# Optimization experiments

Hardware: AMD Instinct MI355X
Metric: run time of the kernel (lower is better)

## Reference

```python
import jax, jax.numpy as jnp
import numpy as np

SEQ = 4096
VOCAB = 50257
IN = 1024
HID = 1024


def setup_inputs() -> dict:
    key = jax.random.key(0)
    ks = jax.random.split(key, 8)
    s = 1.0 / np.sqrt(HID).astype(np.float32)
    inputs = jax.random.randint(ks[0], (SEQ,), 0, VOCAB)
    emb = jax.random.normal(ks[1], (VOCAB, IN), jnp.float32) * 0.02
    W_ih = jax.random.uniform(ks[2], (4 * HID, IN), jnp.float32, -s, s)
    W_hh = jax.random.uniform(ks[3], (4 * HID, HID), jnp.float32, -s, s)
    b_ih = jax.random.uniform(ks[4], (4 * HID,), jnp.float32, -s, s)
    b_hh = jax.random.uniform(ks[5], (4 * HID,), jnp.float32, -s, s)
    h0 = jax.random.normal(ks[6], (HID,), jnp.float32)
    c0 = jax.random.normal(ks[7], (HID,), jnp.float32)
    return {"inputs": inputs, "emb": emb, "W_ih": W_ih, "W_hh": W_hh,
            "b_ih": b_ih, "b_hh": b_hh, "h0": h0, "c0": c0}


def _lstm_last_hidden(inputs, emb, W_ih, W_hh, b_ih, b_hh, h0, c0):
    # Embed all tokens, then precompute the input-side gate projections in
    # one big GEMM: [S, 4H]. (Fuses the per-timestep x @ W_ih.T of torch.)
    x = emb[inputs]                      # [S, IN]
    xg = x @ W_ih.T + (b_ih + b_hh)      # [S, 4H]

    def step(carry, xg_t):
        h, c = carry
        g = xg_t + W_hh @ h              # [4H], PyTorch gate order i,f,g,o
        i, f, gg, o = jnp.split(g, 4)
        i = jax.nn.sigmoid(i)
        f = jax.nn.sigmoid(f)
        gg = jnp.tanh(gg)
        o = jax.nn.sigmoid(o)
        c = f * c + i * gg
        h = o * jnp.tanh(c)
        return (h, c), None

    (h, _), _ = jax.lax.scan(step, (h0, c0), xg)
    return h                              # [HID] = out of last timestep


def reference(inputs, emb, W_ih, W_hh, b_ih, b_hh, h0, c0):
    h = _lstm_last_hidden(inputs, emb, W_ih, W_hh, b_ih, b_hh, h0, c0)
    # scores = F.log_softmax(out.view(1, -1), dim=1) -> [1, HID]
    return jax.nn.log_softmax(h[None, :], axis=1)
```

## Files before the change

kernel.cpp:

```cpp
#include <hip/hip_runtime.h>
#include <cmath>

#define SEQ   4096
#define INP   1024
#define HID   1024
#define G4    4096

__global__ __launch_bounds__(256) void xg_gemm_kernel(
    const int* __restrict__ inputs,
    const float* __restrict__ emb,
    const float* __restrict__ W_ih,
    const float* __restrict__ b_ih,
    const float* __restrict__ b_hh,
    float* __restrict__ xg)
{
    __shared__ __align__(16) float As[16][68];
    __shared__ __align__(16) float Bs[16][68];
    __shared__ int toks[64];

    const int tid = threadIdx.x;
    const int bt = blockIdx.y * 64;
    const int br = blockIdx.x * 64;

    if (tid < 64) toks[tid] = inputs[bt + tid];
    __syncthreads();

    const int tx = tid & 15;
    const int ty = tid >> 4;
    const int si = tid >> 2;
    const int sk = (tid & 3) * 4;

    float acc[4][4] = {};

    for (int kk = 0; kk < INP; kk += 16) {
        float4 av = *(const float4*)(emb  + (size_t)toks[si] * INP + kk + sk);
        float4 bv = *(const float4*)(W_ih + (size_t)(br + si) * INP + kk + sk);
        As[sk+0][si] = av.x; As[sk+1][si] = av.y; As[sk+2][si] = av.z; As[sk+3][si] = av.w;
        Bs[sk+0][si] = bv.x; Bs[sk+1][si] = bv.y; Bs[sk+2][si] = bv.z; Bs[sk+3][si] = bv.w;
        __syncthreads();
        #pragma unroll
        for (int k = 0; k < 16; ++k) {
            float4 a = *(const float4*)&As[k][ty * 4];
            float4 b = *(const float4*)&Bs[k][tx * 4];
            float ar[4] = {a.x, a.y, a.z, a.w};
            float brr[4] = {b.x, b.y, b.z, b.w};
            #pragma unroll
            for (int iy = 0; iy < 4; ++iy)
                #pragma unroll
                for (int ix = 0; ix < 4; ++ix)
                    acc[iy][ix] += ar[iy] * brr[ix];
        }
        __syncthreads();
    }

    const int r0 = br + tx * 4;
    float4 bias;
    bias.x = b_ih[r0+0] + b_hh[r0+0];
    bias.y = b_ih[r0+1] + b_hh[r0+1];
    bias.z = b_ih[r0+2] + b_hh[r0+2];
    bias.w = b_ih[r0+3] + b_hh[r0+3];
    #pragma unroll
    for (int iy = 0; iy < 4; ++iy) {
        float4 o;
        o.x = acc[iy][0] + bias.x;
        o.y = acc[iy][1] + bias.y;
        o.z = acc[iy][2] + bias.z;
        o.w = acc[iy][3] + bias.w;
        *(float4*)(xg + (size_t)(bt + ty * 4 + iy) * G4 + r0) = o;
    }
}

__device__ __forceinline__ float fast_sigmoid(float x) {
    x = fminf(fmaxf(x, -30.f), 30.f);
    return __builtin_amdgcn_rcpf(1.0f + __expf(-x));
}
__device__ __forceinline__ float fast_tanh(float x) {
    x = fminf(fmaxf(x, -15.f), 15.f);
    float e = __expf(2.0f * x);
    return (e - 1.0f) * __builtin_amdgcn_rcpf(e + 1.0f);
}

__device__ __forceinline__ unsigned long long mb_load(const unsigned long long* p) {
    return __hip_atomic_load(p, __ATOMIC_RELAXED, __HIP_MEMORY_SCOPE_AGENT);
}

template <int CTRL>
__device__ __forceinline__ float dpp_mov(float x) {
    return __int_as_float(__builtin_amdgcn_update_dpp(
        0, __float_as_int(x), CTRL, 0xF, 0xF, true));
}

__global__ __launch_bounds__(1024, 4) void lstm_kernel(
    const float* __restrict__ xg,
    const float* __restrict__ W_hh,
    const float* __restrict__ h0,
    const float* __restrict__ c0,
    unsigned long long* __restrict__ hbuf,
    float* __restrict__ out)
{
    const int w    = blockIdx.x;
    const int tid  = threadIdx.x;
    const int lane = tid & 63;
    const int wv   = tid >> 6;
    const int qq   = lane >> 4;
    const int kc   = lane & 15;
    const int j    = w * 16 + wv;

    float wreg[4][16];
    {
        #pragma unroll
        for (int q = 0; q < 4; ++q) {
            const float* wp = W_hh + (size_t)(q * HID + j) * HID + kc * 64 + qq * 16;
            #pragma unroll
            for (int m = 0; m < 4; ++m) {
                float4 v = *(const float4*)(wp + 4 * m);
                wreg[q][4*m+0] = v.x; wreg[q][4*m+1] = v.y;
                wreg[q][4*m+2] = v.z; wreg[q][4*m+3] = v.w;
            }
        }
    }

    float c = c0[j];

    if (wv == 0 && lane < 16) {
        unsigned long long pk =
            (unsigned long long)__float_as_uint(h0[w * 16 + lane]);
        __hip_atomic_store(hbuf + w * 16 + lane, pk,
                           __ATOMIC_RELAXED, __HIP_MEMORY_SCOPE_AGENT);
    }

    __shared__ __align__(16) float hs[16 * 68];
    __shared__ float xgs[64];
    __shared__ float hout[16];

    const int lofs = (tid >> 6) * 68 + (tid & 63);
    const bool hasx = (tid < 64);
    const size_t xgofs = (size_t)(tid >> 4) * HID + w * 16 + (tid & 15);
    const float* hp = hs + kc * 68 + qq * 16;

    for (int t = 0; t < SEQ; ++t) {
        const int par = t & 1;
        const unsigned long long* slot = hbuf + (size_t)par * 1024 + tid;

        float xv = 0.f;
        if (hasx) xv = xg[(size_t)t * G4 + xgofs];

        const unsigned int tg = (unsigned int)t;
        unsigned long long v;
        {
            unsigned long long p0 = mb_load(slot);
            unsigned long long p1 = mb_load(slot);
            unsigned long long p2 = mb_load(slot);
            unsigned long long p3 = mb_load(slot);
            for (;;) {
                if ((unsigned int)(p0 >> 32) == tg) { v = p0; break; }
                p0 = mb_load(slot);
                if ((unsigned int)(p1 >> 32) == tg) { v = p1; break; }
                p1 = mb_load(slot);
                if ((unsigned int)(p2 >> 32) == tg) { v = p2; break; }
                p2 = mb_load(slot);
                if ((unsigned int)(p3 >> 32) == tg) { v = p3; break; }
                p3 = mb_load(slot);
            }
        }

        hs[lofs] = __uint_as_float((unsigned int)v);
        if (hasx) xgs[tid] = xv;
        __syncthreads();

        float p[4] = {0.f, 0.f, 0.f, 0.f};
        #pragma unroll
        for (int m = 0; m < 4; ++m) {
            float4 hv = *(const float4*)(hp + 4 * m);
            #pragma unroll
            for (int q = 0; q < 4; ++q) {
                p[q] += wreg[q][4*m+0] * hv.x;
                p[q] += wreg[q][4*m+1] * hv.y;
                p[q] += wreg[q][4*m+2] * hv.z;
                p[q] += wreg[q][4*m+3] * hv.w;
            }
        }

        #pragma unroll
        for (int q = 0; q < 4; ++q) {
            p[q] += dpp_mov<0xB1>(p[q]);
            p[q] += dpp_mov<0x4E>(p[q]);
            p[q] += dpp_mov<0x124>(p[q]);
            p[q] += dpp_mov<0x128>(p[q]);
            p[q] += __shfl_xor(p[q], 16);
            p[q] += __shfl_xor(p[q], 32);
        }

        float gi = p[0] + xgs[ 0 + wv];
        float gf = p[1] + xgs[16 + wv];
        float gg = p[2] + xgs[32 + wv];
        float go = p[3] + xgs[48 + wv];

        float ig = fast_sigmoid(gi);
        float fg = fast_sigmoid(gf);
        float gc = fast_tanh(gg);
        float og = fast_sigmoid(go);
        c = fg * c + ig * gc;
        float h = og * fast_tanh(c);

        if (lane == 0) hout[wv] = h;
        __syncthreads();

        if (wv == 0 && lane < 16) {
            unsigned long long pk =
                ((unsigned long long)(unsigned int)(t + 1) << 32) |
                (unsigned long long)__float_as_uint(hout[lane]);
            __hip_atomic_store(
                hbuf + (size_t)((t + 1) & 1) * 1024 + w * 16 + lane, pk,
                __ATOMIC_RELAXED, __HIP_MEMORY_SCOPE_AGENT);
        }
    }

    if (w != 0) return;

    float a;
    {
        const unsigned int tg = (unsigned int)SEQ;
        const unsigned long long* slot = hbuf + tid;
        unsigned long long v;
        do {
            v = mb_load(slot);
        } while ((unsigned int)(v >> 32) != tg);
        a = __uint_as_float((unsigned int)v);
    }

    __shared__ float rmax[16];
    __shared__ float rsum[16];

    float lm = a;
    #pragma unroll
    for (int d = 1; d < 64; d <<= 1) lm = fmaxf(lm, __shfl_xor(lm, d));
    if (lane == 0) rmax[wv] = lm;
    __syncthreads();
    float gm = rmax[0];
    #pragma unroll
    for (int i = 1; i < 16; ++i) gm = fmaxf(gm, rmax[i]);

    float ls = expf(a - gm);
    #pragma unroll
    for (int d = 1; d < 64; d <<= 1) ls += __shfl_xor(ls, d);
    if (lane == 0) rsum[wv] = ls;
    __syncthreads();
    float tot = rsum[0];
    #pragma unroll
    for (int i = 1; i < 16; ++i) tot += rsum[i];
    const float lse = gm + logf(tot);

    out[tid] = a - lse;
}

extern "C" void kernel_launch(void* const* d_in, const int* in_sizes, int n_in,
                              void* d_out, int out_size, void* d_ws, size_t ws_size,
                              hipStream_t stream)
{
    const int*   inputs = (const int*)d_in[0];
    const float* emb    = (const float*)d_in[1];
    const float* W_ih   = (const float*)d_in[2];
    const float* W_hh   = (const float*)d_in[3];
    const float* b_ih   = (const float*)d_in[4];
    const float* b_hh   = (const float*)d_in[5];
    const float* h0     = (const float*)d_in[6];
    const float* c0     = (const float*)d_in[7];
    float* out = (float*)d_out;

    float* xg = (float*)d_ws;
    unsigned long long* hbuf =
        (unsigned long long*)((char*)d_ws + (size_t)SEQ * G4 * sizeof(float));

    dim3 g1(G4 / 64, SEQ / 64), b1(256);
    hipLaunchKernelGGL(xg_gemm_kernel, g1, b1, 0, stream,
                       inputs, emb, W_ih, b_ih, b_hh, xg);

    void* args[] = { (void*)&xg, (void*)&W_hh, (void*)&h0, (void*)&c0,
                     (void*)&hbuf, (void*)&out };
    hipLaunchCooperativeKernel((void*)lstm_kernel, dim3(64), dim3(1024),
                               args, 0u, stream);
}
```

Before: 9.456 ms.

## Spread LSTM recurrence over 256 small blocks with double-buffered smem and one barrier

The persistent recurrent kernel moves from 64 blocks of 1024 threads (16 hidden units each) to 256 blocks of 256 threads (4 hidden units each). Each thread now polls four hbuf slots and stages h into shared memory. The shared h and xg buffers are double-buffered by step parity, so the second __syncthreads per step is dropped and each wave publishes its own h. The aim is shorter block-wide barriers and more CUs working on the matvec, at the cost of more blocks polling global memory and more polling per thread.

```diff
diff --git a/kernel.cpp b/kernel.cpp
--- a/kernel.cpp
+++ b/kernel.cpp
@@ -90,7 +90,7 @@
         0, __float_as_int(x), CTRL, 0xF, 0xF, true));
 }
 
-__global__ __launch_bounds__(1024, 4) void lstm_kernel(
+__global__ __launch_bounds__(256, 1) void lstm_kernel(
     const float* __restrict__ xg,
     const float* __restrict__ W_hh,
     const float* __restrict__ h0,
@@ -104,7 +104,14 @@
     const int wv   = tid >> 6;
     const int qq   = lane >> 4;
     const int kc   = lane & 15;
-    const int j    = w * 16 + wv;
+    const int j    = w * 4 + wv;
+
+    if (lane == 0) {
+        unsigned long long pk =
+            (unsigned long long)__float_as_uint(h0[j]);
+        __hip_atomic_store(hbuf + j, pk,
+                           __ATOMIC_RELAXED, __HIP_MEMORY_SCOPE_AGENT);
+    }
 
     float wreg[4][16];
     {
@@ -122,21 +129,12 @@
 
     float c = c0[j];
 
-    if (wv == 0 && lane < 16) {
-        unsigned long long pk =
-            (unsigned long long)__float_as_uint(h0[w * 16 + lane]);
-        __hip_atomic_store(hbuf + w * 16 + lane, pk,
-                           __ATOMIC_RELAXED, __HIP_MEMORY_SCOPE_AGENT);
-    }
-
-    __shared__ __align__(16) float hs[16 * 68];
-    __shared__ float xgs[64];
-    __shared__ float hout[16];
-
-    const int lofs = (tid >> 6) * 68 + (tid & 63);
-    const bool hasx = (tid < 64);
-    const size_t xgofs = (size_t)(tid >> 4) * HID + w * 16 + (tid & 15);
-    const float* hp = hs + kc * 68 + qq * 16;
+    __shared__ __align__(16) float hs[2][16 * 68];
+    __shared__ float xgs[2][16];
+
+    const int wofs = (tid >> 6) * 68 + (tid & 63);
+    const bool hasx = (tid < 16);
+    const size_t xgofs = (size_t)(tid >> 2) * HID + w * 4 + (tid & 3);
 
     for (int t = 0; t < SEQ; ++t) {
         const int par = t & 1;
@@ -146,28 +144,27 @@
         if (hasx) xv = xg[(size_t)t * G4 + xgofs];
 
         const unsigned int tg = (unsigned int)t;
-        unsigned long long v;
-        {
-            unsigned long long p0 = mb_load(slot);
-            unsigned long long p1 = mb_load(slot);
-            unsigned long long p2 = mb_load(slot);
-            unsigned long long p3 = mb_load(slot);
-            for (;;) {
-                if ((unsigned int)(p0 >> 32) == tg) { v = p0; break; }
-                p0 = mb_load(slot);
-                if ((unsigned int)(p1 >> 32) == tg) { v = p1; break; }
-                p1 = mb_load(slot);
-                if ((unsigned int)(p2 >> 32) == tg) { v = p2; break; }
-                p2 = mb_load(slot);
-                if ((unsigned int)(p3 >> 32) == tg) { v = p3; break; }
-                p3 = mb_load(slot);
-            }
-        }
-
-        hs[lofs] = __uint_as_float((unsigned int)v);
-        if (hasx) xgs[tid] = xv;
+        unsigned long long a0 = mb_load(slot);
+        unsigned long long a1 = mb_load(slot + 256);
+        unsigned long long a2 = mb_load(slot + 512);
+        unsigned long long a3 = mb_load(slot + 768);
+        unsigned mOK = 0u;
+        while (mOK != 15u) {
+            if (!(mOK & 1u)) { if ((unsigned)(a0 >> 32) == tg) mOK |= 1u; else a0 = mb_load(slot);       }
+            if (!(mOK & 2u)) { if ((unsigned)(a1 >> 32) == tg) mOK |= 2u; else a1 = mb_load(slot + 256); }
+            if (!(mOK & 4u)) { if ((unsigned)(a2 >> 32) == tg) mOK |= 4u; else a2 = mb_load(slot + 512); }
+            if (!(mOK & 8u)) { if ((unsigned)(a3 >> 32) == tg) mOK |= 8u; else a3 = mb_load(slot + 768); }
+        }
+
+        float* hb = hs[par];
+        hb[wofs           ] = __uint_as_float((unsigned)a0);
+        hb[wofs +  4 * 68 ] = __uint_as_float((unsigned)a1);
+        hb[wofs +  8 * 68 ] = __uint_as_float((unsigned)a2);
+        hb[wofs + 12 * 68 ] = __uint_as_float((unsigned)a3);
+        if (hasx) xgs[par][tid] = xv;
         __syncthreads();
 
+        const float* hp = hb + kc * 68 + qq * 16;
         float p[4] = {0.f, 0.f, 0.f, 0.f};
         #pragma unroll
         for (int m = 0; m < 4; ++m) {
@@ -191,10 +188,10 @@
             p[q] += __shfl_xor(p[q], 32);
         }
 
-        float gi = p[0] + xgs[ 0 + wv];
-        float gf = p[1] + xgs[16 + wv];
-        float gg = p[2] + xgs[32 + wv];
-        float go = p[3] + xgs[48 + wv];
+        float gi = p[0] + xgs[par][ 0 + wv];
+        float gf = p[1] + xgs[par][ 4 + wv];
+        float gg = p[2] + xgs[par][ 8 + wv];
+        float go = p[3] + xgs[par][12 + wv];
 
         float ig = fast_sigmoid(gi);
         float fg = fast_sigmoid(gf);
@@ -203,55 +200,79 @@
         c = fg * c + ig * gc;
         float h = og * fast_tanh(c);
 
-        if (lane == 0) hout[wv] = h;
-        __syncthreads();
-
-        if (wv == 0 && lane < 16) {
+        if (lane == 0) {
             unsigned long long pk =
                 ((unsigned long long)(unsigned int)(t + 1) << 32) |
-                (unsigned long long)__float_as_uint(hout[lane]);
+                (unsigned long long)__float_as_uint(h);
             __hip_atomic_store(
-                hbuf + (size_t)((t + 1) & 1) * 1024 + w * 16 + lane, pk,
+                hbuf + (size_t)((t + 1) & 1) * 1024 + j, pk,
                 __ATOMIC_RELAXED, __HIP_MEMORY_SCOPE_AGENT);
         }
     }
 
     if (w != 0) return;
 
-    float a;
+    const unsigned int tgf = (unsigned int)SEQ;
+    float a0, a1, a2, a3;
     {
-        const unsigned int tg = (unsigned int)SEQ;
-        const unsigned long long* slot = hbuf + tid;
         unsigned long long v;
-        do {
-            v = mb_load(slot);
-        } while ((unsigned int)(v >> 32) != tg);
-        a = __uint_as_float((unsigned int)v);
+        do { v = mb_load(hbuf + tid);       } while ((unsigned)(v >> 32) != tgf);
+        a0 = __uint_as_float((unsigned)v);
+        do { v = mb_load(hbuf + tid + 256); } while ((unsigned)(v >> 32) != tgf);
+        a1 = __uint_as_float((unsigned)v);
+        do { v = mb_load(hbuf + tid + 512); } while ((unsigned)(v >> 32) != tgf);
+        a2 = __uint_as_float((unsigned)v);
+        do { v = mb_load(hbuf + tid + 768); } while ((unsigned)(v >> 32) != tgf);
+        a3 = __uint_as_float((unsigned)v);
     }
 
     __shared__ float rmax[16];
     __shared__ float rsum[16];
 
-    float lm = a;
-    #pragma unroll
-    for (int d = 1; d < 64; d <<= 1) lm = fmaxf(lm, __shfl_xor(lm, d));
-    if (lane == 0) rmax[wv] = lm;
+    float m0 = a0, m1 = a1, m2 = a2, m3 = a3;
+    #pragma unroll
+    for (int d = 1; d < 64; d <<= 1) {
+        m0 = fmaxf(m0, __shfl_xor(m0, d));
+        m1 = fmaxf(m1, __shfl_xor(m1, d));
+        m2 = fmaxf(m2, __shfl_xor(m2, d));
+        m3 = fmaxf(m3, __shfl_xor(m3, d));
+    }
+    if (lane == 0) {
+        rmax[wv +  0] = m0;
+        rmax[wv +  4] = m1;
+        rmax[wv +  8] = m2;
+        rmax[wv + 12] = m3;
+    }
     __syncthreads();
     float gm = rmax[0];
     #pragma unroll
     for (int i = 1; i < 16; ++i) gm = fmaxf(gm, rmax[i]);
 
-    float ls = expf(a - gm);
-    #pragma unroll
-    for (int d = 1; d < 64; d <<= 1) ls += __shfl_xor(ls, d);
-    if (lane == 0) rsum[wv] = ls;
+    float s0 = expf(a0 - gm), s1 = expf(a1 - gm);
+    float s2 = expf(a2 - gm), s3 = expf(a3 - gm);
+    #pragma unroll
+    for (int d = 1; d < 64; d <<= 1) {
+        s0 += __shfl_xor(s0, d);
+        s1 += __shfl_xor(s1, d);
+        s2 += __shfl_xor(s2, d);
+        s3 += __shfl_xor(s3, d);
+    }
+    if (lane == 0) {
+        rsum[wv +  0] = s0;
+        rsum[wv +  4] = s1;
+        rsum[wv +  8] = s2;
+        rsum[wv + 12] = s3;
+    }
     __syncthreads();
     float tot = rsum[0];
     #pragma unroll
     for (int i = 1; i < 16; ++i) tot += rsum[i];
     const float lse = gm + logf(tot);
 
-    out[tid] = a - lse;
+    out[tid      ] = a0 - lse;
+    out[tid + 256] = a1 - lse;
+    out[tid + 512] = a2 - lse;
+    out[tid + 768] = a3 - lse;
 }
 
 extern "C" void kernel_launch(void* const* d_in, const int* in_sizes, int n_in,
@@ -278,6 +299,6 @@
 
     void* args[] = { (void*)&xg, (void*)&W_hh, (void*)&h0, (void*)&c0,
                      (void*)&hbuf, (void*)&out };
-    hipLaunchCooperativeKernel((void*)lstm_kernel, dim3(64), dim3(1024),
+    hipLaunchCooperativeKernel((void*)lstm_kernel, dim3(256), dim3(256),
                                args, 0u, stream);
 }
```

New measurement: 15.43 ms. +63.2%, slower.

## Fuse input GEMM into recurrent kernel with per-chunk producer/consumer flags

Applied to the files above, without the earlier changes.

Merges the input-projection GEMM and the LSTM recurrence into a single cooperative launch of 256 workgroups. 192 workgroups compute xg tiles chunk by chunk and bump a per-64-timestep counter, while 64 workgroups run the recurrence and spin on that counter before consuming each chunk. This overlaps the GEMM with the serial recurrence and removes a kernel launch boundary. The recurrent matvec also switches to packed 2-wide float math on paired gate rows. The cost is extra spin-waiting and a dependence on all 256 workgroups being co-resident.

```diff
diff --git a/kernel.cpp b/kernel.cpp
--- a/kernel.cpp
+++ b/kernel.cpp
@@ -6,117 +6,145 @@
 #define HID   1024
 #define G4    4096
 
-__global__ __launch_bounds__(256) void xg_gemm_kernel(
-    const int* __restrict__ inputs,
+typedef float f32x2 __attribute__((ext_vector_type(2)));
+
+__device__ __forceinline__ float fast_sigmoid(float x) {
+    x = fminf(fmaxf(x, -30.f), 30.f);
+    return __builtin_amdgcn_rcpf(1.0f + __expf(-x));
+}
+__device__ __forceinline__ float fast_tanh(float x) {
+    x = fminf(fmaxf(x, -15.f), 15.f);
+    float e = __expf(2.0f * x);
+    return (e - 1.0f) * __builtin_amdgcn_rcpf(e + 1.0f);
+}
+
+__device__ __forceinline__ unsigned long long mb_load(const unsigned long long* p) {
+    return __hip_atomic_load(p, __ATOMIC_RELAXED, __HIP_MEMORY_SCOPE_AGENT);
+}
+
+template <int CTRL>
+__device__ __forceinline__ float dpp_mov(float x) {
+    return __int_as_float(__builtin_amdgcn_update_dpp(
+        0, __float_as_int(x), CTRL, 0xF, 0xF, true));
+}
+
+__global__ __launch_bounds__(1024, 4) void fused_kernel(
+    const int*   __restrict__ inputs,
     const float* __restrict__ emb,
     const float* __restrict__ W_ih,
     const float* __restrict__ b_ih,
     const float* __restrict__ b_hh,
-    float* __restrict__ xg)
-{
-    __shared__ __align__(16) float As[16][68];
-    __shared__ __align__(16) float Bs[16][68];
-    __shared__ int toks[64];
-
-    const int tid = threadIdx.x;
-    const int bt = blockIdx.y * 64;
-    const int br = blockIdx.x * 64;
-
-    if (tid < 64) toks[tid] = inputs[bt + tid];
-    __syncthreads();
-
-    const int tx = tid & 15;
-    const int ty = tid >> 4;
-    const int si = tid >> 2;
-    const int sk = (tid & 3) * 4;
-
-    float acc[4][4] = {};
-
-    for (int kk = 0; kk < INP; kk += 16) {
-        float4 av = *(const float4*)(emb  + (size_t)toks[si] * INP + kk + sk);
-        float4 bv = *(const float4*)(W_ih + (size_t)(br + si) * INP + kk + sk);
-        As[sk+0][si] = av.x; As[sk+1][si] = av.y; As[sk+2][si] = av.z; As[sk+3][si] = av.w;
-        Bs[sk+0][si] = bv.x; Bs[sk+1][si] = bv.y; Bs[sk+2][si] = bv.z; Bs[sk+3][si] = bv.w;
-        __syncthreads();
-        #pragma unroll
-        for (int k = 0; k < 16; ++k) {
-            float4 a = *(const float4*)&As[k][ty * 4];
-            float4 b = *(const float4*)&Bs[k][tx * 4];
-            float ar[4] = {a.x, a.y, a.z, a.w};
-            float brr[4] = {b.x, b.y, b.z, b.w};
-            #pragma unroll
-            for (int iy = 0; iy < 4; ++iy)
-                #pragma unroll
-                for (int ix = 0; ix < 4; ++ix)
-                    acc[iy][ix] += ar[iy] * brr[ix];
-        }
-        __syncthreads();
-    }
-
-    const int r0 = br + tx * 4;
-    float4 bias;
-    bias.x = b_ih[r0+0] + b_hh[r0+0];
-    bias.y = b_ih[r0+1] + b_hh[r0+1];
-    bias.z = b_ih[r0+2] + b_hh[r0+2];
-    bias.w = b_ih[r0+3] + b_hh[r0+3];
-    #pragma unroll
-    for (int iy = 0; iy < 4; ++iy) {
-        float4 o;
-        o.x = acc[iy][0] + bias.x;
-        o.y = acc[iy][1] + bias.y;
-        o.z = acc[iy][2] + bias.z;
-        o.w = acc[iy][3] + bias.w;
-        *(float4*)(xg + (size_t)(bt + ty * 4 + iy) * G4 + r0) = o;
-    }
-}
-
-__device__ __forceinline__ float fast_sigmoid(float x) {
-    x = fminf(fmaxf(x, -30.f), 30.f);
-    return __builtin_amdgcn_rcpf(1.0f + __expf(-x));
-}
-__device__ __forceinline__ float fast_tanh(float x) {
-    x = fminf(fmaxf(x, -15.f), 15.f);
-    float e = __expf(2.0f * x);
-    return (e - 1.0f) * __builtin_amdgcn_rcpf(e + 1.0f);
-}
-
-__device__ __forceinline__ unsigned long long mb_load(const unsigned long long* p) {
-    return __hip_atomic_load(p, __ATOMIC_RELAXED, __HIP_MEMORY_SCOPE_AGENT);
-}
-
-template <int CTRL>
-__device__ __forceinline__ float dpp_mov(float x) {
-    return __int_as_float(__builtin_amdgcn_update_dpp(
-        0, __float_as_int(x), CTRL, 0xF, 0xF, true));
-}
-
-__global__ __launch_bounds__(1024, 4) void lstm_kernel(
-    const float* __restrict__ xg,
     const float* __restrict__ W_hh,
     const float* __restrict__ h0,
     const float* __restrict__ c0,
+    float*       __restrict__ xg,
     unsigned long long* __restrict__ hbuf,
-    float* __restrict__ out)
+    int*         __restrict__ xgcnt,
+    float*       __restrict__ out)
 {
-    const int w    = blockIdx.x;
-    const int tid  = threadIdx.x;
+    const int w   = blockIdx.x;
+    const int tid = threadIdx.x;
+
+    if (w >= 64) {
+        __shared__ __align__(16) float As[4][16][68];
+        __shared__ __align__(16) float Bs[4][16][68];
+        __shared__ int toks[4][64];
+
+        const int wgP = w - 64;
+        const int sb  = tid >> 8;
+        const int t2  = tid & 255;
+        const int tx  = t2 & 15;
+        const int ty  = t2 >> 4;
+        const int si  = t2 >> 2;
+        const int sk  = (t2 & 3) * 4;
+
+        for (int it = 0; it < 6; ++it) {
+            const int Q   = wgP + 192 * it;
+            const bool act = (Q < 1024);
+            const int g   = Q * 4 + sb;
+            const int bt  = (g >> 6) * 64;
+            const int br  = (g & 63) * 64;
+
+            if (act && t2 < 64) toks[sb][t2] = inputs[bt + t2];
+            __syncthreads();
+
+            float acc[4][4] = {};
+            for (int kk = 0; kk < INP; kk += 16) {
+                if (act) {
+                    float4 av = *(const float4*)(emb  + (size_t)toks[sb][si] * INP + kk + sk);
+                    float4 bv = *(const float4*)(W_ih + (size_t)(br + si) * INP + kk + sk);
+                    As[sb][sk+0][si] = av.x; As[sb][sk+1][si] = av.y;
+                    As[sb][sk+2][si] = av.z; As[sb][sk+3][si] = av.w;
+                    Bs[sb][sk+0][si] = bv.x; Bs[sb][sk+1][si] = bv.y;
+                    Bs[sb][sk+2][si] = bv.z; Bs[sb][sk+3][si] = bv.w;
+                }
+                __syncthreads();
+                if (act) {
+                    #pragma unroll
+                    for (int k = 0; k < 16; ++k) {
+                        float4 a = *(const float4*)&As[sb][k][ty * 4];
+                        float4 b = *(const float4*)&Bs[sb][k][tx * 4];
+                        float ar[4] = {a.x, a.y, a.z, a.w};
+                        float brr[4] = {b.x, b.y, b.z, b.w};
+                        #pragma unroll
+                        for (int iy = 0; iy < 4; ++iy)
+                            #pragma unroll
+                            for (int ix = 0; ix < 4; ++ix)
+                                acc[iy][ix] += ar[iy] * brr[ix];
+                    }
+                }
+                __syncthreads();
+            }
+
+            if (act) {
+                const int r0 = br + tx * 4;
+                float4 bias;
+                bias.x = b_ih[r0+0] + b_hh[r0+0];
+                bias.y = b_ih[r0+1] + b_hh[r0+1];
+                bias.z = b_ih[r0+2] + b_hh[r0+2];
+                bias.w = b_ih[r0+3] + b_hh[r0+3];
+                #pragma unroll
+                for (int iy = 0; iy < 4; ++iy) {
+                    float4 o;
+                    o.x = acc[iy][0] + bias.x;
+                    o.y = acc[iy][1] + bias.y;
+                    o.z = acc[iy][2] + bias.z;
+                    o.w = acc[iy][3] + bias.w;
+                    *(float4*)(xg + (size_t)(bt + ty * 4 + iy) * G4 + r0) = o;
+                }
+            }
+            __syncthreads();
+            if (act && t2 == 0) {
+                __threadfence();
+                atomicAdd(xgcnt + (g >> 6), 1);
+            }
+        }
+        return;
+    }
+
     const int lane = tid & 63;
     const int wv   = tid >> 6;
     const int qq   = lane >> 4;
     const int kc   = lane & 15;
     const int j    = w * 16 + wv;
 
-    float wreg[4][16];
+    f32x2 wp01[16], wp23[16];
     {
+        const int o = kc * 64 + qq * 16;
+        const float* r0p = W_hh + (size_t)(0 * HID + j) * HID + o;
+        const float* r1p = W_hh + (size_t)(1 * HID + j) * HID + o;
+        const float* r2p = W_hh + (size_t)(2 * HID + j) * HID + o;
+        const float* r3p = W_hh + (size_t)(3 * HID + j) * HID + o;
         #pragma unroll
-        for (int q = 0; q < 4; ++q) {
-            const float* wp = W_hh + (size_t)(q * HID + j) * HID + kc * 64 + qq * 16;
-            #pragma unroll
-            for (int m = 0; m < 4; ++m) {
-                float4 v = *(const float4*)(wp + 4 * m);
-                wreg[q][4*m+0] = v.x; wreg[q][4*m+1] = v.y;
-                wreg[q][4*m+2] = v.z; wreg[q][4*m+3] = v.w;
-            }
+        for (int m = 0; m < 4; ++m) {
+            float4 a0 = *(const float4*)(r0p + 4 * m);
+            float4 a1 = *(const float4*)(r1p + 4 * m);
+            float4 a2 = *(const float4*)(r2p + 4 * m);
+            float4 a3 = *(const float4*)(r3p + 4 * m);
+            wp01[4*m+0] = (f32x2){a0.x, a1.x}; wp23[4*m+0] = (f32x2){a2.x, a3.x};
+            wp01[4*m+1] = (f32x2){a0.y, a1.y}; wp23[4*m+1] = (f32x2){a2.y, a3.y};
+            wp01[4*m+2] = (f32x2){a0.z, a1.z}; wp23[4*m+2] = (f32x2){a2.z, a3.z};
+            wp01[4*m+3] = (f32x2){a0.w, a1.w}; wp23[4*m+3] = (f32x2){a2.w, a3.w};
         }
     }
 
@@ -141,6 +169,11 @@
     for (int t = 0; t < SEQ; ++t) {
         const int par = t & 1;
         const unsigned long long* slot = hbuf + (size_t)par * 1024 + tid;
+
+        if ((t & 63) == 0) {
+            while (__hip_atomic_load(xgcnt + (t >> 6), __ATOMIC_ACQUIRE,
+                                     __HIP_MEMORY_SCOPE_AGENT) != 64) {}
+        }
 
         float xv = 0.f;
         if (hasx) xv = xg[(size_t)t * G4 + xgofs];
@@ -168,18 +201,18 @@
         if (hasx) xgs[tid] = xv;
         __syncthreads();
 
-        float p[4] = {0.f, 0.f, 0.f, 0.f};
+        f32x2 p01 = {0.f, 0.f}, p23 = {0.f, 0.f};
         #pragma unroll
         for (int m = 0; m < 4; ++m) {
             float4 hv = *(const float4*)(hp + 4 * m);
-            #pragma unroll
-            for (int q = 0; q < 4; ++q) {
-                p[q] += wreg[q][4*m+0] * hv.x;
-                p[q] += wreg[q][4*m+1] * hv.y;
-                p[q] += wreg[q][4*m+2] * hv.z;
-                p[q] += wreg[q][4*m+3] * hv.w;
-            }
-        }
+            f32x2 h0v = {hv.x, hv.x}, h1v = {hv.y, hv.y};
+            f32x2 h2v = {hv.z, hv.z}, h3v = {hv.w, hv.w};
+            p01 += wp01[4*m+0] * h0v;  p23 += wp23[4*m+0] * h0v;
+            p01 += wp01[4*m+1] * h1v;  p23 += wp23[4*m+1] * h1v;
+            p01 += wp01[4*m+2] * h2v;  p23 += wp23[4*m+2] * h2v;
+            p01 += wp01[4*m+3] * h3v;  p23 += wp23[4*m+3] * h3v;
+        }
+        float p[4] = {p01.x, p01.y, p23.x, p23.y};
 
         #pragma unroll
         for (int q = 0; q < 4; ++q) {
@@ -268,16 +301,19 @@
     const float* c0     = (const float*)d_in[7];
     float* out = (float*)d_out;
 
+    const size_t XG_BYTES   = (size_t)SEQ * G4 * sizeof(float);
+    const size_t HBUF_BYTES = 2 * 1024 * sizeof(unsigned long long);
     float* xg = (float*)d_ws;
     unsigned long long* hbuf =
-        (unsigned long long*)((char*)d_ws + (size_t)SEQ * G4 * sizeof(float));
-
-    dim3 g1(G4 / 64, SEQ / 64), b1(256);
-    hipLaunchKernelGGL(xg_gemm_kernel, g1, b1, 0, stream,
-                       inputs, emb, W_ih, b_ih, b_hh, xg);
-
-    void* args[] = { (void*)&xg, (void*)&W_hh, (void*)&h0, (void*)&c0,
-                     (void*)&hbuf, (void*)&out };
-    hipLaunchCooperativeKernel((void*)lstm_kernel, dim3(64), dim3(1024),
+        (unsigned long long*)((char*)d_ws + XG_BYTES);
+    int* xgcnt = (int*)((char*)d_ws + XG_BYTES + HBUF_BYTES);
+
+    hipMemsetAsync(xgcnt, 0, 64 * sizeof(int), stream);
+
+    void* args[] = { (void*)&inputs, (void*)&emb, (void*)&W_ih,
+                     (void*)&b_ih, (void*)&b_hh, (void*)&W_hh,
+                     (void*)&h0, (void*)&c0,
+                     (void*)&xg, (void*)&hbuf, (void*)&xgcnt, (void*)&out };
+    hipLaunchCooperativeKernel((void*)fused_kernel, dim3(256), dim3(1024),
                                args, 0u, stream);
 }
```

Result: slower. 9.908 ms (+4.8%).

## Halve LSTM block size, two hidden units per wave with packed float2 FMAs

Applied to the files above, without the earlier changes.

The recurrent kernel now runs 512 threads per block instead of 1024, with each wave computing two hidden units. Weights are held as float2 pairs so the matvec can use packed FMA instructions, and each thread polls two mailbox slots. The aim is to shorten the per-step __syncthreads and barrier latency and raise FMA throughput on the serial critical path. In exchange, register pressure doubles per thread and the reductions plus gate math per wave double.

```diff
diff --git a/kernel.cpp b/kernel.cpp
--- a/kernel.cpp
+++ b/kernel.cpp
@@ -5,6 +5,8 @@
 #define INP   1024
 #define HID   1024
 #define G4    4096
+
+typedef float f32x2 __attribute__((ext_vector_type(2)));
 
 __global__ __launch_bounds__(256) void xg_gemm_kernel(
     const int* __restrict__ inputs,
@@ -90,7 +92,7 @@
         0, __float_as_int(x), CTRL, 0xF, 0xF, true));
 }
 
-__global__ __launch_bounds__(1024, 4) void lstm_kernel(
+__global__ __launch_bounds__(512, 2) void lstm_kernel(
     const float* __restrict__ xg,
     const float* __restrict__ W_hh,
     const float* __restrict__ h0,
@@ -104,23 +106,10 @@
     const int wv   = tid >> 6;
     const int qq   = lane >> 4;
     const int kc   = lane & 15;
-    const int j    = w * 16 + wv;
-
-    float wreg[4][16];
-    {
-        #pragma unroll
-        for (int q = 0; q < 4; ++q) {
-            const float* wp = W_hh + (size_t)(q * HID + j) * HID + kc * 64 + qq * 16;
-            #pragma unroll
-            for (int m = 0; m < 4; ++m) {
-                float4 v = *(const float4*)(wp + 4 * m);
-                wreg[q][4*m+0] = v.x; wreg[q][4*m+1] = v.y;
-                wreg[q][4*m+2] = v.z; wreg[q][4*m+3] = v.w;
-            }
-        }
-    }
-
-    float c = c0[j];
+    const int ww0  = 2 * wv;
+    const int ww1  = ww0 + 1;
+    const int j0   = w * 16 + ww0;
+    const int j1   = j0 + 1;
 
     if (wv == 0 && lane < 16) {
         unsigned long long pk =
@@ -129,60 +118,100 @@
                            __ATOMIC_RELAXED, __HIP_MEMORY_SCOPE_AGENT);
     }
 
+    f32x2 wA01[16], wA23[16], wB01[16], wB23[16];
+    {
+        const int o = kc * 64 + qq * 16;
+        const float* r0A = W_hh + (size_t)(0 * HID + j0) * HID + o;
+        const float* r1A = W_hh + (size_t)(1 * HID + j0) * HID + o;
+        const float* r2A = W_hh + (size_t)(2 * HID + j0) * HID + o;
+        const float* r3A = W_hh + (size_t)(3 * HID + j0) * HID + o;
+        const float* r0B = W_hh + (size_t)(0 * HID + j1) * HID + o;
+        const float* r1B = W_hh + (size_t)(1 * HID + j1) * HID + o;
+        const float* r2B = W_hh + (size_t)(2 * HID + j1) * HID + o;
+        const float* r3B = W_hh + (size_t)(3 * HID + j1) * HID + o;
+        #pragma unroll
+        for (int m = 0; m < 4; ++m) {
+            float4 a0 = *(const float4*)(r0A + 4 * m);
+            float4 a1 = *(const float4*)(r1A + 4 * m);
+            float4 a2 = *(const float4*)(r2A + 4 * m);
+            float4 a3 = *(const float4*)(r3A + 4 * m);
+            wA01[4*m+0] = (f32x2){a0.x, a1.x}; wA23[4*m+0] = (f32x2){a2.x, a3.x};
+            wA01[4*m+1] = (f32x2){a0.y, a1.y}; wA23[4*m+1] = (f32x2){a2.y, a3.y};
+            wA01[4*m+2] = (f32x2){a0.z, a1.z}; wA23[4*m+2] = (f32x2){a2.z, a3.z};
+            wA01[4*m+3] = (f32x2){a0.w, a1.w}; wA23[4*m+3] = (f32x2){a2.w, a3.w};
+            float4 b0 = *(const float4*)(r0B + 4 * m);
+            float4 b1 = *(const float4*)(r1B + 4 * m);
+            float4 b2 = *(const float4*)(r2B + 4 * m);
+            float4 b3 = *(const float4*)(r3B + 4 * m);
+            wB01[4*m+0] = (f32x2){b0.x, b1.x}; wB23[4*m+0] = (f32x2){b2.x, b3.x};
+            wB01[4*m+1] = (f32x2){b0.y, b1.y}; wB23[4*m+1] = (f32x2){b2.y, b3.y};
+            wB01[4*m+2] = (f32x2){b0.z, b1.z}; wB23[4*m+2] = (f32x2){b2.z, b3.z};
+            wB01[4*m+3] = (f32x2){b0.w, b1.w}; wB23[4*m+3] = (f32x2){b2.w, b3.w};
+        }
+    }
+
+    float cA = c0[j0];
+    float cB = c0[j1];
+
     __shared__ __align__(16) float hs[16 * 68];
     __shared__ float xgs[64];
     __shared__ float hout[16];
 
-    const int lofs = (tid >> 6) * 68 + (tid & 63);
+    const int lofsA = (tid >> 6) * 68 + (tid & 63);
+    const int lofsB = (8 + (tid >> 6)) * 68 + (tid & 63);
     const bool hasx = (tid < 64);
     const size_t xgofs = (size_t)(tid >> 4) * HID + w * 16 + (tid & 15);
     const float* hp = hs + kc * 68 + qq * 16;
 
     for (int t = 0; t < SEQ; ++t) {
         const int par = t & 1;
-        const unsigned long long* slot = hbuf + (size_t)par * 1024 + tid;
+        const unsigned long long* s0 = hbuf + (size_t)par * 1024 + tid;
+        const unsigned long long* s1 = s0 + 512;
 
         float xv = 0.f;
         if (hasx) xv = xg[(size_t)t * G4 + xgofs];
 
         const unsigned int tg = (unsigned int)t;
-        unsigned long long v;
+        unsigned long long v0, v1;
         {
-            unsigned long long p0 = mb_load(slot);
-            unsigned long long p1 = mb_load(slot);
-            unsigned long long p2 = mb_load(slot);
-            unsigned long long p3 = mb_load(slot);
+            unsigned long long p0 = mb_load(s0), q0 = mb_load(s0);
+            unsigned long long p1 = mb_load(s1), q1 = mb_load(s1);
+            unsigned ok = 0;
             for (;;) {
-                if ((unsigned int)(p0 >> 32) == tg) { v = p0; break; }
-                p0 = mb_load(slot);
-                if ((unsigned int)(p1 >> 32) == tg) { v = p1; break; }
-                p1 = mb_load(slot);
-                if ((unsigned int)(p2 >> 32) == tg) { v = p2; break; }
-                p2 = mb_load(slot);
-                if ((unsigned int)(p3 >> 32) == tg) { v = p3; break; }
-                p3 = mb_load(slot);
+                if (!(ok & 1u)) { if ((unsigned)(p0 >> 32) == tg) { v0 = p0; ok |= 1u; } else p0 = mb_load(s0); }
+                if (!(ok & 2u)) { if ((unsigned)(p1 >> 32) == tg) { v1 = p1; ok |= 2u; } else p1 = mb_load(s1); }
+                if (ok == 3u) break;
+                if (!(ok & 1u)) { if ((unsigned)(q0 >> 32) == tg) { v0 = q0; ok |= 1u; } else q0 = mb_load(s0); }
+                if (!(ok & 2u)) { if ((unsigned)(q1 >> 32) == tg) { v1 = q1; ok |= 2u; } else q1 = mb_load(s1); }
+                if (ok == 3u) break;
             }
         }
 
-        hs[lofs] = __uint_as_float((unsigned int)v);
+        hs[lofsA] = __uint_as_float((unsigned)v0);
+        hs[lofsB] = __uint_as_float((unsigned)v1);
         if (hasx) xgs[tid] = xv;
         __syncthreads();
 
-        float p[4] = {0.f, 0.f, 0.f, 0.f};
+        f32x2 pA01 = {0.f, 0.f}, pA23 = {0.f, 0.f};
+        f32x2 pB01 = {0.f, 0.f}, pB23 = {0.f, 0.f};
         #pragma unroll
         for (int m = 0; m < 4; ++m) {
             float4 hv = *(const float4*)(hp + 4 * m);
+            float hvs[4] = {hv.x, hv.y, hv.z, hv.w};
             #pragma unroll
-            for (int q = 0; q < 4; ++q) {
-                p[q] += wreg[q][4*m+0] * hv.x;
-                p[q] += wreg[q][4*m+1] * hv.y;
-                p[q] += wreg[q][4*m+2] * hv.z;
-                p[q] += wreg[q][4*m+3] * hv.w;
+            for (int s = 0; s < 4; ++s) {
+                f32x2 hb = {hvs[s], hvs[s]};
+                pA01 += wA01[4*m+s] * hb;
+                pA23 += wA23[4*m+s] * hb;
+                pB01 += wB01[4*m+s] * hb;
+                pB23 += wB23[4*m+s] * hb;
             }
         }
+        float p[8] = {pA01.x, pA01.y, pA23.x, pA23.y,
+                      pB01.x, pB01.y, pB23.x, pB23.y};
 
         #pragma unroll
-        for (int q = 0; q < 4; ++q) {
+        for (int q = 0; q < 8; ++q) {
             p[q] += dpp_mov<0xB1>(p[q]);
             p[q] += dpp_mov<0x4E>(p[q]);
             p[q] += dpp_mov<0x124>(p[q]);
@@ -191,19 +220,30 @@
             p[q] += __shfl_xor(p[q], 32);
         }
 
-        float gi = p[0] + xgs[ 0 + wv];
-        float gf = p[1] + xgs[16 + wv];
-        float gg = p[2] + xgs[32 + wv];
-        float go = p[3] + xgs[48 + wv];
-
-        float ig = fast_sigmoid(gi);
-        float fg = fast_sigmoid(gf);
-        float gc = fast_tanh(gg);
-        float og = fast_sigmoid(go);
-        c = fg * c + ig * gc;
-        float h = og * fast_tanh(c);
-
-        if (lane == 0) hout[wv] = h;
+        float giA = p[0] + xgs[ 0 + ww0];
+        float gfA = p[1] + xgs[16 + ww0];
+        float ggA = p[2] + xgs[32 + ww0];
+        float goA = p[3] + xgs[48 + ww0];
+        float giB = p[4] + xgs[ 0 + ww1];
+        float gfB = p[5] + xgs[16 + ww1];
+        float ggB = p[6] + xgs[32 + ww1];
+        float goB = p[7] + xgs[48 + ww1];
+
+        float igA = fast_sigmoid(giA);
+        float fgA = fast_sigmoid(gfA);
+        float gcA = fast_tanh(ggA);
+        float ogA = fast_sigmoid(goA);
+        cA = fgA * cA + igA * gcA;
+        float hA = ogA * fast_tanh(cA);
+
+        float igB = fast_sigmoid(giB);
+        float fgB = fast_sigmoid(gfB);
+        float gcB = fast_tanh(ggB);
+        float ogB = fast_sigmoid(goB);
+        cB = fgB * cB + igB * gcB;
+        float hB = ogB * fast_tanh(cB);
+
+        if (lane == 0) { hout[ww0] = hA; hout[ww1] = hB; }
         __syncthreads();
 
         if (wv == 0 && lane < 16) {
@@ -218,40 +258,52 @@
 
     if (w != 0) return;
 
-    float a;
+    const unsigned int tgf = (unsigned int)SEQ;
+    float a0, a1;
     {
-        const unsigned int tg = (unsigned int)SEQ;
-        const unsigned long long* slot = hbuf + tid;
         unsigned long long v;
-        do {
-            v = mb_load(slot);
-        } while ((unsigned int)(v >> 32) != tg);
-        a = __uint_as_float((unsigned int)v);
+        do { v = mb_load(hbuf + tid);       } while ((unsigned)(v >> 32) != tgf);
+        a0 = __uint_as_float((unsigned)v);
+        do { v = mb_load(hbuf + tid + 512); } while ((unsigned)(v >> 32) != tgf);
+        a1 = __uint_as_float((unsigned)v);
     }
 
     __shared__ float rmax[16];
     __shared__ float rsum[16];
 
-    float lm = a;
-    #pragma unroll
-    for (int d = 1; d < 64; d <<= 1) lm = fmaxf(lm, __shfl_xor(lm, d));
-    if (lane == 0) rmax[wv] = lm;
+    float m0 = a0, m1 = a1;
+    #pragma unroll
+    for (int d = 1; d < 64; d <<= 1) {
+        m0 = fmaxf(m0, __shfl_xor(m0, d));
+        m1 = fmaxf(m1, __shfl_xor(m1, d));
+    }
+    if (lane == 0) {
+        rmax[wv    ] = m0;
+        rmax[wv + 8] = m1;
+    }
     __syncthreads();
     float gm = rmax[0];
     #pragma unroll
     for (int i = 1; i < 16; ++i) gm = fmaxf(gm, rmax[i]);
 
-    float ls = expf(a - gm);
-    #pragma unroll
-    for (int d = 1; d < 64; d <<= 1) ls += __shfl_xor(ls, d);
-    if (lane == 0) rsum[wv] = ls;
+    float s0 = expf(a0 - gm), s1 = expf(a1 - gm);
+    #pragma unroll
+    for (int d = 1; d < 64; d <<= 1) {
+        s0 += __shfl_xor(s0, d);
+        s1 += __shfl_xor(s1, d);
+    }
+    if (lane == 0) {
+        rsum[wv    ] = s0;
+        rsum[wv + 8] = s1;
+    }
     __syncthreads();
     float tot = rsum[0];
     #pragma unroll
     for (int i = 1; i < 16; ++i) tot += rsum[i];
     const float lse = gm + logf(tot);
 
-    out[tid] = a - lse;
+    out[tid      ] = a0 - lse;
+    out[tid + 512] = a1 - lse;
 }
 
 extern "C" void kernel_launch(void* const* d_in, const int* in_sizes, int n_in,
@@ -278,6 +330,6 @@
 
     void* args[] = { (void*)&xg, (void*)&W_hh, (void*)&h0, (void*)&c0,
                      (void*)&hbuf, (void*)&out };
-    hipLaunchCooperativeKernel((void*)lstm_kernel, dim3(64), dim3(1024),
+    hipLaunchCooperativeKernel((void*)lstm_kernel, dim3(64), dim3(512),
                                args, 0u, stream);
 }
```

Result: slower. 10.95 ms (+15.8%).
